# Kernel optimization log

Measured on AMD Instinct MI355X. Metric: run time of the kernel, lower is better.

The kernel has to match this reference:

```python
import jax, jax.numpy as jnp
import numpy as np

NUM_HEADS = 4

def setup_inputs() -> dict:
    key = jax.random.key(0)
    k1, k2, k3, k4 = jax.random.split(key, 4)
    B, N, D = 8, 768, 2048
    x = jax.random.normal(k1, (B, N, D), dtype=jnp.float32)
    s = 1.0 / np.sqrt(N)
    W_qk = jax.random.normal(k2, (N, N), dtype=jnp.float32) * s
    W_v = jax.random.normal(k3, (N, N), dtype=jnp.float32) * s
    W_out = jax.random.normal(k4, (N, N), dtype=jnp.float32) * s
    return {"x": x, "W_qk": W_qk, "W_v": W_v, "W_out": W_out}

def reference(x, W_qk, W_v, W_out):
    B, N, D = x.shape
    H = NUM_HEADS
    n = N // H
    y = jnp.swapaxes(x, 1, 2)                    # (B, D, N): attention over channels D
    qk = y @ W_qk.T                              # (B, D, N)
    v = y @ W_v.T                                # (B, D, N)
    # to heads: (B, D, N) -> (B, H, D, n)
    qk = jnp.swapaxes(qk.reshape(B, D, H, n), 1, 2)
    v = jnp.swapaxes(v.reshape(B, D, H, n), 1, 2)
    dot = jnp.einsum('bhdn,bhen->bhde', qk, qk)  # (B, H, D, D)
    q2 = jnp.sum(qk * qk, axis=-1)               # (B, H, D)
    # negative squared Euclidean distance logits: 2*q.k - ||q||^2 - ||k||^2
    logits = 2.0 * dot - q2[..., :, None] - q2[..., None, :]
    attn = jax.nn.softmax(logits, axis=-1)
    w = jnp.einsum('bhde,bhen->bhdn', attn, v)   # (B, H, D, n)
    # from heads: (B, H, D, n) -> (B, D, N)
    w = jnp.swapaxes(w, 1, 2).reshape(B, D, N)
    out = w @ W_out.T                            # (B, D, N)
    return jnp.swapaxes(out, 1, 2)               # (B, N, D)
```

## Files before the change

### kernel.cpp

```cpp
#include <hip/hip_runtime.h>
#include <stdint.h>

#define B_  8
#define N_  768
#define D_  2048
#define H_  4
#define HN  192

#define QROW 200
#define VROW 72
#define KTILE_B 25600
#define VTILE_B 27648
#define KV_CHUNKS 3328
#define K_CHUNKS  1600

#define LOG2E 1.4426950408889634f
#define C2    2.8853901617f

typedef unsigned short u16;
typedef float    f32x4 __attribute__((ext_vector_type(4)));
typedef __bf16   bf16x8 __attribute__((ext_vector_type(8)));
typedef __bf16   bf16x4 __attribute__((ext_vector_type(4)));
typedef uint32_t u32x4 __attribute__((ext_vector_type(4)));
typedef uint32_t u32x2 __attribute__((ext_vector_type(2)));

__device__ __forceinline__ u16 f2bf(float f) {
  return __builtin_bit_cast(u16, (__bf16)f);
}

typedef const __attribute__((address_space(1))) void* gas_ptr;
typedef __attribute__((address_space(3))) void* las_ptr;
__device__ __forceinline__ void gld16(const void* g, void* l) {
  __builtin_amdgcn_global_load_lds((gas_ptr)g, (las_ptr)l, 16, 0, 0);
}

__global__ __launch_bounds__(256) void prep(const float* __restrict__ x,
                                            const float* __restrict__ Wqk,
                                            const float* __restrict__ Wv,
                                            const float* __restrict__ Wout,
                                            u16* __restrict__ xt,
                                            u16* __restrict__ oqk,
                                            u16* __restrict__ ov,
                                            u16* __restrict__ oout,
                                            float* __restrict__ q2) {
  __shared__ float tile[64][65];
  const int bid = blockIdx.x;
  const int t   = threadIdx.x;
  if (bid < 3072) {
    const int d0 = (bid & 31) * 64;
    const int n0 = ((bid >> 5) % 12) * 64;
    const int b  = (bid >> 5) / 12;
    const int col = t & 63;
    const int rb  = (t >> 6) * 16;
    const float* src = x + ((size_t)b * N_ + n0) * D_ + d0;
    #pragma unroll
    for (int i = 0; i < 16; i++)
      tile[rb + i][col] = src[(size_t)(rb + i) * D_ + col];
    __syncthreads();
    u16* dst = xt + ((size_t)b * D_ + d0) * N_ + n0;
    #pragma unroll
    for (int i = 0; i < 16; i++)
      dst[(size_t)(rb + i) * N_ + col] = f2bf(tile[col][rb + i]);
  } else if (bid < 4800) {
    const int r   = bid - 3072;
    const int mat = r / 576;
    const float* src = (mat == 0) ? Wqk : ((mat == 1) ? Wv : Wout);
    u16*         dst = (mat == 0) ? oqk : ((mat == 1) ? ov : oout);
    const int i = ((r % 576) * 256 + t) * 4;
    f32x4 v = *(const f32x4*)(src + i);
    bf16x4 tmp;
    #pragma unroll
    for (int j = 0; j < 4; j++) tmp[j] = (__bf16)v[j];
    *(bf16x4*)(dst + i) = tmp;
  } else {
    const f32x4 fz = {0.f, 0.f, 0.f, 0.f};
    const int i = ((bid - 4800) * 256 + t) * 4;
    *(f32x4*)(q2 + i) = fz;
  }
}

__global__ __launch_bounds__(256, 2) void qkv_gemm(const u16* __restrict__ xt,
                                                   const u16* __restrict__ wqk,
                                                   const u16* __restrict__ wv,
                                                   u16* __restrict__ qkb,
                                                   u16* __restrict__ vtb,
                                                   float* __restrict__ q2) {
  const int b     = blockIdx.z;
  const int dtile = blockIdx.x;
  const int d0    = dtile * 128;
  const int j0    = blockIdx.y * 128;
  const int tid  = threadIdx.x;
  const int wave = tid >> 6, lane = tid & 63;
  const int l15  = lane & 15, quad = lane >> 4;
  const int wm = wave >> 1, wn = wave & 1;

  __shared__ u16 At[128 * 32];
  __shared__ u16 Bq[128 * 32];
  __shared__ u16 Bv[128 * 32];

  const f32x4 fz = {0.f, 0.f, 0.f, 0.f};
  f32x4 accq[4][4];
  f32x4 accv[4][4];
  #pragma unroll
  for (int i = 0; i < 4; i++)
    #pragma unroll
    for (int j = 0; j < 4; j++) { accq[i][j] = fz; accv[i][j] = fz; }

  const int srow  = tid >> 2;
  const int sbyte = (tid & 3) * 16;
  const u16* ax = xt  + ((size_t)b * D_ + d0 + srow) * N_;
  const u16* bq = wqk + (size_t)(j0 + srow) * N_;
  const u16* bv = wv  + (size_t)(j0 + srow) * N_;

  for (int k0 = 0; k0 < N_; k0 += 32) {
    __syncthreads();
    #pragma unroll
    for (int c = 0; c < 2; c++) {
      gld16((const char*)(ax + (size_t)c * 64 * N_ + k0) + sbyte,
            (char*)At + c * 4096 + tid * 16);
      gld16((const char*)(bq + (size_t)c * 64 * N_ + k0) + sbyte,
            (char*)Bq + c * 4096 + tid * 16);
      gld16((const char*)(bv + (size_t)c * 64 * N_ + k0) + sbyte,
            (char*)Bv + c * 4096 + tid * 16);
    }
    __syncthreads();

    bf16x8 Af[4];
    #pragma unroll
    for (int mi = 0; mi < 4; mi++)
      Af[mi] = *(const bf16x8*)&At[(wm * 64 + mi * 16 + l15) * 32 + quad * 8];
    #pragma unroll
    for (int ni = 0; ni < 4; ni++) {
      bf16x8 Bqf = *(const bf16x8*)&Bq[(wn * 64 + ni * 16 + l15) * 32 + quad * 8];
      bf16x8 Bvf = *(const bf16x8*)&Bv[(wn * 64 + ni * 16 + l15) * 32 + quad * 8];
      #pragma unroll
      for (int mi = 0; mi < 4; mi++) {
        accq[ni][mi] = __builtin_amdgcn_mfma_f32_16x16x32_bf16(Bqf, Af[mi], accq[ni][mi], 0, 0, 0);
        accv[mi][ni] = __builtin_amdgcn_mfma_f32_16x16x32_bf16(Af[mi], Bvf, accv[mi][ni], 0, 0, 0);
      }
    }
  }

  const int h_w  = (j0 + wn * 64) / HN;
  const int jn_w = (j0 + wn * 64) % HN;
  const size_t bh = (size_t)b * H_ + h_w;

  #pragma unroll
  for (int md = 0; md < 4; md++) {
    float s = 0.f;
    #pragma unroll
    for (int nj = 0; nj < 4; nj++)
      #pragma unroll
      for (int r = 0; r < 4; r++) { float v = accq[nj][md][r]; s += v * v; }
    s += __shfl_xor(s, 16, 64);
    s += __shfl_xor(s, 32, 64);
    if (quad == 0)
      atomicAdd(&q2[bh * D_ + d0 + wm * 64 + md * 16 + l15], s * LOG2E);
  }

  u16* qtbase = qkb + bh * (size_t)(D_ * QROW);
  #pragma unroll
  for (int md = 0; md < 4; md++) {
    const size_t dro = (size_t)(d0 + wm * 64 + md * 16 + l15) * QROW;
    #pragma unroll
    for (int nj = 0; nj < 4; nj++) {
      bf16x4 tmp;
      #pragma unroll
      for (int r = 0; r < 4; r++) tmp[r] = (__bf16)accq[nj][md][r];
      *(bf16x4*)(qtbase + dro + jn_w + nj * 16 + quad * 4) = tmp;
    }
  }

  const int etile = dtile * 2 + wm;
  u16* vtbase = vtb + bh * (size_t)(32 * HN * VROW) + (size_t)etile * (HN * VROW);
  #pragma unroll
  for (int ni = 0; ni < 4; ni++) {
    const size_t jro = (size_t)(jn_w + ni * 16 + l15) * VROW;
    #pragma unroll
    for (int mi = 0; mi < 4; mi++) {
      bf16x4 tmp;
      #pragma unroll
      for (int r = 0; r < 4; r++) tmp[r] = (__bf16)accv[mi][ni][r];
      *(bf16x4*)(vtbase + jro + mi * 16 + quad * 4) = tmp;
    }
  }
}

__global__ __launch_bounds__(256, 2) void attn_kernel(const u16* __restrict__ qkb,
                                                      const u16* __restrict__ vtb,
                                                      const float* __restrict__ q2,
                                                      u16* __restrict__ wbuf) {
  const int bid  = blockIdx.x;
  const int bh   = (bid & 7) * 4 + (bid >> 7);
  const int dblk = (bid >> 3) & 15;
  const int b = bh >> 2, h = bh & 3;
  const int tid  = threadIdx.x;
  const int wave = tid >> 6, lane = tid & 63;
  const int l15  = lane & 15, quad = lane >> 4;

  __shared__ u16 KV[(KTILE_B + VTILE_B) / 2];
  __shared__ u16 Plds[4][32][VROW];
  u16* Klds = KV;
  u16* Vlds = KV + KTILE_B / 2;

  const u16* kg = qkb + (size_t)bh * (D_ * QROW);
  const u16* vg = vtb + (size_t)bh * (32 * HN * VROW);
  const float* q2g = q2 + (size_t)bh * D_;

  bf16x8 Qf[2][6];
  {
    const u16* qrow = kg + (size_t)(dblk * 128 + wave * 32 + l15) * QROW + quad * 8;
    #pragma unroll
    for (int nt = 0; nt < 2; nt++)
      #pragma unroll
      for (int f = 0; f < 6; f++)
        Qf[nt][f] = *(const bf16x8*)(qrow + (size_t)nt * 16 * QROW + f * 32);
  }
  float cd[2];
  cd[0] = q2g[dblk * 128 + wave * 32 + l15];
  cd[1] = q2g[dblk * 128 + wave * 32 + 16 + l15];

  bf16x8 OnesF;
  #pragma unroll
  for (int j = 0; j < 8; j++) OnesF[j] = (__bf16)1.0f;

  const f32x4 fz = {0.f, 0.f, 0.f, 0.f};
  f32x4 O[2][12];
  f32x4 Or[2];
  #pragma unroll
  for (int mt = 0; mt < 2; mt++) {
    Or[mt] = fz;
    #pragma unroll
    for (int c = 0; c < 12; c++) O[mt][c] = fz;
  }

  u32x4 stg[13];
  #define LOADT(T)                                                            \
    {                                                                         \
      const char* kgt = (const char*)kg + (size_t)(T) * KTILE_B;              \
      const char* vgt = (const char*)vg + (size_t)(T) * VTILE_B;              \
      _Pragma("unroll")                                                       \
      for (int i = 0; i < 13; i++) {                                          \
        const int c = tid + 256 * i;                                          \
        const char* src = (c < K_CHUNKS) ? (kgt + (size_t)c * 16)             \
                                         : (vgt + (size_t)(c - K_CHUNKS) * 16); \
        stg[i] = *(const u32x4*)src;                                          \
      }                                                                       \
    }

  LOADT(0);

  for (int t = 0; t < 32; t++) {
    __syncthreads();
    #pragma unroll
    for (int i = 0; i < 13; i++)
      *(u32x4*)((char*)KV + (size_t)(tid + 256 * i) * 16) = stg[i];
    __syncthreads();
    if (t < 31) LOADT(t + 1);

    #pragma unroll
    for (int et = 0; et < 4; et++) {
      bf16x8 Kf[6];
      #pragma unroll
      for (int f = 0; f < 6; f++)
        Kf[f] = *(const bf16x8*)&Klds[(et * 16 + l15) * QROW + f * 32 + quad * 8];
      f32x4 S0 = fz, S1 = fz;
      __builtin_amdgcn_s_setprio(1);
      #pragma unroll
      for (int f = 0; f < 6; f++) {
        S0 = __builtin_amdgcn_mfma_f32_16x16x32_bf16(Kf[f], Qf[0][f], S0, 0, 0, 0);
        S1 = __builtin_amdgcn_mfma_f32_16x16x32_bf16(Kf[f], Qf[1][f], S1, 0, 0, 0);
      }
      __builtin_amdgcn_s_setprio(0);
      const f32x4 ce = *(const f32x4*)&q2g[t * 64 + et * 16 + quad * 4];
      bf16x4 pb0, pb1;
      #pragma unroll
      for (int r = 0; r < 4; r++) {
        float p0 = __builtin_amdgcn_exp2f(__builtin_fmaf(S0[r], C2, -(ce[r] + cd[0])));
        float p1 = __builtin_amdgcn_exp2f(__builtin_fmaf(S1[r], C2, -(ce[r] + cd[1])));
        pb0[r] = (__bf16)p0;
        pb1[r] = (__bf16)p1;
      }
      *(bf16x4*)&Plds[wave][l15][et * 16 + quad * 4]      = pb0;
      *(bf16x4*)&Plds[wave][16 + l15][et * 16 + quad * 4] = pb1;
    }

    #pragma unroll
    for (int kk = 0; kk < 2; kk++) {
      bf16x8 Pf0 = *(const bf16x8*)&Plds[wave][l15][kk * 32 + quad * 8];
      bf16x8 Pf1 = *(const bf16x8*)&Plds[wave][16 + l15][kk * 32 + quad * 8];
      __builtin_amdgcn_s_setprio(1);
      #pragma unroll
      for (int c = 0; c < 12; c++) {
        bf16x8 Vf = *(const bf16x8*)&Vlds[(c * 16 + l15) * VROW + kk * 32 + quad * 8];
        O[0][c] = __builtin_amdgcn_mfma_f32_16x16x32_bf16(Pf0, Vf, O[0][c], 0, 0, 0);
        O[1][c] = __builtin_amdgcn_mfma_f32_16x16x32_bf16(Pf1, Vf, O[1][c], 0, 0, 0);
      }
      Or[0] = __builtin_amdgcn_mfma_f32_16x16x32_bf16(Pf0, OnesF, Or[0], 0, 0, 0);
      Or[1] = __builtin_amdgcn_mfma_f32_16x16x32_bf16(Pf1, OnesF, Or[1], 0, 0, 0);
      __builtin_amdgcn_s_setprio(0);
    }
  }

  #pragma unroll
  for (int mt = 0; mt < 2; mt++)
    #pragma unroll
    for (int r = 0; r < 4; r++) {
      const float inv = __builtin_amdgcn_rcpf(Or[mt][r]);
      const int d = dblk * 128 + wave * 32 + mt * 16 + quad * 4 + r;
      u16* wrow = wbuf + ((size_t)b * D_ + d) * N_ + h * HN;
      #pragma unroll
      for (int c = 0; c < 12; c++)
        wrow[c * 16 + l15] = f2bf(O[mt][c][r] * inv);
    }
}

__global__ __launch_bounds__(256, 2) void out_gemm(const u16* __restrict__ wbuf,
                                                   const u16* __restrict__ wout,
                                                   float* __restrict__ outp) {
  const int b  = blockIdx.z;
  const int d0 = blockIdx.x * 128;
  const int i0 = blockIdx.y * 128;
  const int tid  = threadIdx.x;
  const int wave = tid >> 6, lane = tid & 63;
  const int l15  = lane & 15, quad = lane >> 4;
  const int wm = wave >> 1, wn = wave & 1;

  __shared__ u16 At[128 * 32];
  __shared__ u16 Bt[128 * 32];

  const f32x4 fz = {0.f, 0.f, 0.f, 0.f};
  f32x4 acc[4][4];
  #pragma unroll
  for (int i = 0; i < 4; i++)
    #pragma unroll
    for (int j = 0; j < 4; j++) acc[i][j] = fz;

  const int srow  = tid >> 2;
  const int sbyte = (tid & 3) * 16;
  const u16* ax = wbuf + ((size_t)b * D_ + d0 + srow) * N_;
  const u16* bw = wout + (size_t)(i0 + srow) * N_;

  for (int k0 = 0; k0 < N_; k0 += 32) {
    __syncthreads();
    #pragma unroll
    for (int c = 0; c < 2; c++) {
      gld16((const char*)(ax + (size_t)c * 64 * N_ + k0) + sbyte,
            (char*)At + c * 4096 + tid * 16);
      gld16((const char*)(bw + (size_t)c * 64 * N_ + k0) + sbyte,
            (char*)Bt + c * 4096 + tid * 16);
    }
    __syncthreads();

    bf16x8 Af[4];
    #pragma unroll
    for (int mi = 0; mi < 4; mi++)
      Af[mi] = *(const bf16x8*)&At[(wm * 64 + mi * 16 + l15) * 32 + quad * 8];
    #pragma unroll
    for (int ni = 0; ni < 4; ni++) {
      bf16x8 Bf = *(const bf16x8*)&Bt[(wn * 64 + ni * 16 + l15) * 32 + quad * 8];
      #pragma unroll
      for (int mi = 0; mi < 4; mi++)
        acc[mi][ni] = __builtin_amdgcn_mfma_f32_16x16x32_bf16(Af[mi], Bf, acc[mi][ni], 0, 0, 0);
    }
  }

  #pragma unroll
  for (int ni = 0; ni < 4; ni++) {
    float* orow = outp + ((size_t)b * N_ + i0 + wn * 64 + ni * 16 + l15) * D_
                + d0 + wm * 64 + quad * 4;
    #pragma unroll
    for (int mi = 0; mi < 4; mi++)
      *(f32x4*)(orow + mi * 16) = acc[mi][ni];
  }
}

extern "C" void kernel_launch(void* const* d_in, const int* in_sizes, int n_in,
                              void* d_out, int out_size, void* d_ws, size_t ws_size,
                              hipStream_t stream) {
  (void)in_sizes; (void)n_in; (void)out_size; (void)ws_size;
  const float* x    = (const float*)d_in[0];
  const float* Wqk  = (const float*)d_in[1];
  const float* Wv   = (const float*)d_in[2];
  const float* Wout = (const float*)d_in[3];
  float* outp = (float*)d_out;

  char* ws = (char*)d_ws;
  size_t off = 0;
  u16* xt   = (u16*)(ws + off); off += (size_t)B_ * D_ * N_ * 2;
  u16* qkb  = (u16*)(ws + off); off += (size_t)B_ * H_ * D_ * QROW * 2;
  u16* vtb  = (u16*)(ws + off); off += (size_t)B_ * H_ * 32 * HN * VROW * 2;
  float* q2 = (float*)(ws + off); off += (size_t)B_ * H_ * D_ * 4;
  u16* wqk_bf  = (u16*)(ws + off); off += (size_t)N_ * N_ * 2;
  u16* wv_bf   = (u16*)(ws + off); off += (size_t)N_ * N_ * 2;
  u16* wout_bf = (u16*)(ws + off); off += (size_t)N_ * N_ * 2;
  u16* wbuf = xt;

  prep<<<dim3(4864), 256, 0, stream>>>(x, Wqk, Wv, Wout, xt, wqk_bf, wv_bf, wout_bf, q2);
  qkv_gemm<<<dim3(D_ / 128, N_ / 128, B_), 256, 0, stream>>>(xt, wqk_bf, wv_bf, qkb, vtb, q2);
  attn_kernel<<<dim3((D_ / 128) * B_ * H_), 256, 0, stream>>>(qkb, vtb, q2, wbuf);
  out_gemm<<<dim3(D_ / 128, N_ / 128, B_), 256, 0, stream>>>(wbuf, wout_bf, outp);
}
```

Measured before the change: 335.4 us.

## Widen GEMM K-tiles to 64 and use direct-to-LDS loads in attention

```diff
diff --git a/kernel.cpp b/kernel.cpp
--- a/kernel.cpp
+++ b/kernel.cpp
@@ -11,8 +11,6 @@
 #define VROW 72
 #define KTILE_B 25600
 #define VTILE_B 27648
-#define KV_CHUNKS 3328
-#define K_CHUNKS  1600
 
 #define LOG2E 1.4426950408889634f
 #define C2    2.8853901617f
@@ -94,9 +92,9 @@
   const int l15  = lane & 15, quad = lane >> 4;
   const int wm = wave >> 1, wn = wave & 1;
 
-  __shared__ u16 At[128 * 32];
-  __shared__ u16 Bq[128 * 32];
-  __shared__ u16 Bv[128 * 32];
+  __shared__ u16 At[128 * 64];
+  __shared__ u16 Bq[128 * 64];
+  __shared__ u16 Bv[128 * 64];
 
   const f32x4 fz = {0.f, 0.f, 0.f, 0.f};
   f32x4 accq[4][4];
@@ -106,37 +104,40 @@
     #pragma unroll
     for (int j = 0; j < 4; j++) { accq[i][j] = fz; accv[i][j] = fz; }
 
-  const int srow  = tid >> 2;
-  const int sbyte = (tid & 3) * 16;
+  const int srow  = tid >> 3;
+  const int sbyte = (tid & 7) * 16;
   const u16* ax = xt  + ((size_t)b * D_ + d0 + srow) * N_;
   const u16* bq = wqk + (size_t)(j0 + srow) * N_;
   const u16* bv = wv  + (size_t)(j0 + srow) * N_;
 
-  for (int k0 = 0; k0 < N_; k0 += 32) {
-    __syncthreads();
-    #pragma unroll
-    for (int c = 0; c < 2; c++) {
-      gld16((const char*)(ax + (size_t)c * 64 * N_ + k0) + sbyte,
+  for (int k0 = 0; k0 < N_; k0 += 64) {
+    __syncthreads();
+    #pragma unroll
+    for (int c = 0; c < 4; c++) {
+      gld16((const char*)(ax + (size_t)c * 32 * N_ + k0) + sbyte,
             (char*)At + c * 4096 + tid * 16);
-      gld16((const char*)(bq + (size_t)c * 64 * N_ + k0) + sbyte,
+      gld16((const char*)(bq + (size_t)c * 32 * N_ + k0) + sbyte,
             (char*)Bq + c * 4096 + tid * 16);
-      gld16((const char*)(bv + (size_t)c * 64 * N_ + k0) + sbyte,
+      gld16((const char*)(bv + (size_t)c * 32 * N_ + k0) + sbyte,
             (char*)Bv + c * 4096 + tid * 16);
     }
     __syncthreads();
 
-    bf16x8 Af[4];
-    #pragma unroll
-    for (int mi = 0; mi < 4; mi++)
-      Af[mi] = *(const bf16x8*)&At[(wm * 64 + mi * 16 + l15) * 32 + quad * 8];
-    #pragma unroll
-    for (int ni = 0; ni < 4; ni++) {
-      bf16x8 Bqf = *(const bf16x8*)&Bq[(wn * 64 + ni * 16 + l15) * 32 + quad * 8];
-      bf16x8 Bvf = *(const bf16x8*)&Bv[(wn * 64 + ni * 16 + l15) * 32 + quad * 8];
-      #pragma unroll
-      for (int mi = 0; mi < 4; mi++) {
-        accq[ni][mi] = __builtin_amdgcn_mfma_f32_16x16x32_bf16(Bqf, Af[mi], accq[ni][mi], 0, 0, 0);
-        accv[mi][ni] = __builtin_amdgcn_mfma_f32_16x16x32_bf16(Af[mi], Bvf, accv[mi][ni], 0, 0, 0);
+    #pragma unroll
+    for (int kk = 0; kk < 2; kk++) {
+      bf16x8 Af[4];
+      #pragma unroll
+      for (int mi = 0; mi < 4; mi++)
+        Af[mi] = *(const bf16x8*)&At[(wm * 64 + mi * 16 + l15) * 64 + kk * 32 + quad * 8];
+      #pragma unroll
+      for (int ni = 0; ni < 4; ni++) {
+        bf16x8 Bqf = *(const bf16x8*)&Bq[(wn * 64 + ni * 16 + l15) * 64 + kk * 32 + quad * 8];
+        bf16x8 Bvf = *(const bf16x8*)&Bv[(wn * 64 + ni * 16 + l15) * 64 + kk * 32 + quad * 8];
+        #pragma unroll
+        for (int mi = 0; mi < 4; mi++) {
+          accq[ni][mi] = __builtin_amdgcn_mfma_f32_16x16x32_bf16(Bqf, Af[mi], accq[ni][mi], 0, 0, 0);
+          accv[mi][ni] = __builtin_amdgcn_mfma_f32_16x16x32_bf16(Af[mi], Bvf, accv[mi][ni], 0, 0, 0);
+        }
       }
     }
   }
@@ -198,10 +199,9 @@
   const int wave = tid >> 6, lane = tid & 63;
   const int l15  = lane & 15, quad = lane >> 4;
 
-  __shared__ u16 KV[(KTILE_B + VTILE_B) / 2];
+  __shared__ u16 Klds[64 * QROW];
+  __shared__ u16 Vlds[HN * VROW];
   __shared__ u16 Plds[4][32][VROW];
-  u16* Klds = KV;
-  u16* Vlds = KV + KTILE_B / 2;
 
   const u16* kg = qkb + (size_t)bh * (D_ * QROW);
   const u16* vg = vtb + (size_t)bh * (32 * HN * VROW);
@@ -234,29 +234,19 @@
     for (int c = 0; c < 12; c++) O[mt][c] = fz;
   }
 
-  u32x4 stg[13];
-  #define LOADT(T)                                                            \
-    {                                                                         \
-      const char* kgt = (const char*)kg + (size_t)(T) * KTILE_B;              \
-      const char* vgt = (const char*)vg + (size_t)(T) * VTILE_B;              \
-      _Pragma("unroll")                                                       \
-      for (int i = 0; i < 13; i++) {                                          \
-        const int c = tid + 256 * i;                                          \
-        const char* src = (c < K_CHUNKS) ? (kgt + (size_t)c * 16)             \
-                                         : (vgt + (size_t)(c - K_CHUNKS) * 16); \
-        stg[i] = *(const u32x4*)src;                                          \
-      }                                                                       \
-    }
-
-  LOADT(0);
-
   for (int t = 0; t < 32; t++) {
     __syncthreads();
-    #pragma unroll
-    for (int i = 0; i < 13; i++)
-      *(u32x4*)((char*)KV + (size_t)(tid + 256 * i) * 16) = stg[i];
-    __syncthreads();
-    if (t < 31) LOADT(t + 1);
+    {
+      const char* ks = (const char*)kg + (size_t)t * KTILE_B;
+      char* kd = (char*)Klds;
+      for (int c = wave; c < 25; c += 4)
+        gld16(ks + c * 1024 + lane * 16, kd + c * 1024 + lane * 16);
+      const char* vs = (const char*)vg + (size_t)t * VTILE_B;
+      char* vd = (char*)Vlds;
+      for (int c = wave; c < 27; c += 4)
+        gld16(vs + c * 1024 + lane * 16, vd + c * 1024 + lane * 16);
+    }
+    __syncthreads();
 
     #pragma unroll
     for (int et = 0; et < 4; et++) {
@@ -326,8 +316,8 @@
   const int l15  = lane & 15, quad = lane >> 4;
   const int wm = wave >> 1, wn = wave & 1;
 
-  __shared__ u16 At[128 * 32];
-  __shared__ u16 Bt[128 * 32];
+  __shared__ u16 At[128 * 64];
+  __shared__ u16 Bt[128 * 64];
 
   const f32x4 fz = {0.f, 0.f, 0.f, 0.f};
   f32x4 acc[4][4];
@@ -336,32 +326,35 @@
     #pragma unroll
     for (int j = 0; j < 4; j++) acc[i][j] = fz;
 
-  const int srow  = tid >> 2;
-  const int sbyte = (tid & 3) * 16;
+  const int srow  = tid >> 3;
+  const int sbyte = (tid & 7) * 16;
   const u16* ax = wbuf + ((size_t)b * D_ + d0 + srow) * N_;
   const u16* bw = wout + (size_t)(i0 + srow) * N_;
 
-  for (int k0 = 0; k0 < N_; k0 += 32) {
-    __syncthreads();
-    #pragma unroll
-    for (int c = 0; c < 2; c++) {
-      gld16((const char*)(ax + (size_t)c * 64 * N_ + k0) + sbyte,
+  for (int k0 = 0; k0 < N_; k0 += 64) {
+    __syncthreads();
+    #pragma unroll
+    for (int c = 0; c < 4; c++) {
+      gld16((const char*)(ax + (size_t)c * 32 * N_ + k0) + sbyte,
             (char*)At + c * 4096 + tid * 16);
-      gld16((const char*)(bw + (size_t)c * 64 * N_ + k0) + sbyte,
+      gld16((const char*)(bw + (size_t)c * 32 * N_ + k0) + sbyte,
             (char*)Bt + c * 4096 + tid * 16);
     }
     __syncthreads();
 
-    bf16x8 Af[4];
-    #pragma unroll
-    for (int mi = 0; mi < 4; mi++)
-      Af[mi] = *(const bf16x8*)&At[(wm * 64 + mi * 16 + l15) * 32 + quad * 8];
-    #pragma unroll
-    for (int ni = 0; ni < 4; ni++) {
-      bf16x8 Bf = *(const bf16x8*)&Bt[(wn * 64 + ni * 16 + l15) * 32 + quad * 8];
+    #pragma unroll
+    for (int kk = 0; kk < 2; kk++) {
+      bf16x8 Af[4];
       #pragma unroll
       for (int mi = 0; mi < 4; mi++)
-        acc[mi][ni] = __builtin_amdgcn_mfma_f32_16x16x32_bf16(Af[mi], Bf, acc[mi][ni], 0, 0, 0);
+        Af[mi] = *(const bf16x8*)&At[(wm * 64 + mi * 16 + l15) * 64 + kk * 32 + quad * 8];
+      #pragma unroll
+      for (int ni = 0; ni < 4; ni++) {
+        bf16x8 Bf = *(const bf16x8*)&Bt[(wn * 64 + ni * 16 + l15) * 64 + kk * 32 + quad * 8];
+        #pragma unroll
+        for (int mi = 0; mi < 4; mi++)
+          acc[mi][ni] = __builtin_amdgcn_mfma_f32_16x16x32_bf16(Af[mi], Bf, acc[mi][ni], 0, 0, 0);
+      }
     }
   }
 
```

After: 293.3 us. 1.14x faster.
